# Optimization experiments

Hardware: AMD Instinct MI355X
Metric: run time of the kernel (lower is better)

Reference implementation:

```python
import math
import jax, jax.numpy as jnp
import numpy as np

HIDDEN = 1024   # config.hidden_size
INTER = 4096    # config.intermediate_size
EXPERTS = 8     # config.moe_experts == config.global_experts
B, T = 4, 2048
EPS = 1e-12     # config.epsilon
CAP_FACTOR = 1.0
MIN_CAP = 4


def layer_norm(x, g, b, eps=EPS):
    m = jnp.mean(x, axis=-1, keepdims=True)
    v = jnp.var(x, axis=-1, keepdims=True)
    return (x - m) * jax.lax.rsqrt(v + eps) * g + b


def top1_gate(x, wg, capacity):
    # DeepSpeed top1gating: softmax gate, argmax expert, capacity-based token drop.
    logits = x @ wg                                    # [S, E]
    gates = jax.nn.softmax(logits, axis=-1)
    E = wg.shape[-1]
    idx = jnp.argmax(gates, axis=-1)                   # [S]
    mask1 = jax.nn.one_hot(idx, E, dtype=gates.dtype)  # [S, E]
    locations = jnp.cumsum(mask1, axis=0) - mask1      # exclusive cumsum = slot within expert
    mask1 = mask1 * (locations < capacity).astype(gates.dtype)  # drop overflow tokens
    gates1_s = jnp.sum(gates * mask1, axis=-1)         # [S] prob of chosen expert
    loc_s = jnp.sum(locations * mask1, axis=-1).astype(jnp.int32)
    loc_oh = jax.nn.one_hot(loc_s, capacity, dtype=gates.dtype)          # [S, C]
    combine = gates1_s[:, None, None] * mask1[:, :, None] * loc_oh[:, None, :]  # [S, E, C]
    dispatch = jax.lax.stop_gradient((combine > 0).astype(x.dtype))      # bool mask in torch
    return combine, dispatch


def setup_inputs() -> dict:
    key = jax.random.key(0)
    ks = jax.random.split(key, 8)
    s = 0.02
    return {
        "x": jax.random.normal(ks[0], (B, T, HIDDEN), jnp.float32),
        "attn_nw": jnp.ones((HIDDEN,), jnp.float32),
        "attn_nb": jnp.zeros((HIDDEN,), jnp.float32),
        "wg": jax.random.normal(ks[1], (HIDDEN, EXPERTS), jnp.float32) * s,
        "inter_w": jax.random.normal(ks[2], (EXPERTS, HIDDEN, INTER), jnp.float32) * s,
        "inter_b": jnp.zeros((EXPERTS, INTER), jnp.float32),
        "output_w": jax.random.normal(ks[3], (EXPERTS, INTER, HIDDEN), jnp.float32) * s,
        "output_b": jnp.zeros((EXPERTS, HIDDEN), jnp.float32),
        "res_inter_w": jax.random.normal(ks[4], (HIDDEN, INTER), jnp.float32) * s,
        "res_inter_b": jnp.zeros((INTER,), jnp.float32),
        "res_output_w": jax.random.normal(ks[5], (INTER, HIDDEN), jnp.float32) * s,
        "res_output_b": jnp.zeros((HIDDEN,), jnp.float32),
        "res_coef": jax.random.normal(ks[6], (HIDDEN, 2), jnp.float32) * s,
    }


def reference(x, attn_nw, attn_nb, wg, inter_w, inter_b, output_w, output_b,
              res_inter_w, res_inter_b, res_output_w, res_output_b, res_coef):
    Bx, Tx, M = x.shape
    S = Bx * Tx
    E = wg.shape[-1]
    capacity = max(MIN_CAP, math.ceil(S / E * CAP_FACTOR))  # static

    residual = x.reshape(S, M)                  # attention output + bias (attention = identity here)
    attn_out = layer_norm(residual, attn_nw, attn_nb)  # ds_layernorm

    # gate + dispatch: einsum_sec_sm_ecm
    combine, dispatch = top1_gate(attn_out, wg, capacity)
    dispatched = jnp.einsum('sec,sm->ecm', dispatch, attn_out)  # [E, C, M]

    # expert MLPs: fused gemm-gelu then output projection + bias
    h = jax.nn.gelu(jnp.einsum('ecm,emi->eci', dispatched, inter_w) + inter_b[:, None, :], approximate=True)
    expert_out = jnp.einsum('eci,eim->ecm', h, output_w) + output_b[:, None, :]

    # gated combine: matmul(combine.reshape(S, E*C), expert_out.reshape(E*C, M))
    moe_out = jnp.einsum('sec,ecm->sm', combine, expert_out)

    # residual-MLP branch (mlp_type == 'residual')
    rh = jax.nn.gelu(attn_out @ res_inter_w + res_inter_b, approximate=True)
    res_mlp_out = rh @ res_output_w + res_output_b
    coef = jax.nn.softmax(attn_out @ res_coef, axis=-1)          # [S, 2]
    out = res_mlp_out * coef[:, :1] + moe_out * coef[:, 1:]      # moe_res_matmul

    out = out + residual                                         # bias_residual
    return out.reshape(Bx, Tx, M)
```

## Files before the change

### kernel.cpp

```cpp
#include <hip/hip_runtime.h>
#include <hip/hip_bf16.h>
#include <type_traits>

#define S_TOK 8192
#define HID 1024
#define INTERX 4096
#define NEXP 8
#define CAPX 1024
#define MTOT 16384

using f32x4 = __attribute__((ext_vector_type(4))) float;
using bf16x8 = __attribute__((ext_vector_type(8))) short;

__device__ __forceinline__ short f2bf(float f) {
    union { float f; unsigned u; } v; v.f = f;
    unsigned r = (v.u + 0x7FFFu + ((v.u >> 16) & 1u)) >> 16;
    return (short)r;
}
__device__ __forceinline__ float bflo(int p) {
    union { unsigned u; float f; } v; v.u = (unsigned)p << 16; return v.f;
}
__device__ __forceinline__ float bfhi(int p) {
    union { unsigned u; float f; } v; v.u = (unsigned)p & 0xffff0000u; return v.f;
}

__device__ __forceinline__ float gelu_f(float x) {
    float x2 = x * x;
    float t = __expf(x * fmaf(x2, -0.07135677f, -1.5957691f));
    return x * __builtin_amdgcn_rcpf(1.0f + t);
}

__device__ __forceinline__ void gl_lds16(const short* g, short* l) {
    __builtin_amdgcn_global_load_lds(
        (const __attribute__((address_space(1))) void*)g,
        (__attribute__((address_space(3))) void*)l, 16, 0, 0);
}

template<int PERM>
__device__ __forceinline__ void convtrans_body(
    short (*tile)[72],
    const float* __restrict__ src_e, const float* __restrict__ src_r,
    short* __restrict__ dst, int K, int N, long sSrc, long sDst,
    int bxi, int byi, long z)
{
    const float* s = (z < 8) ? (src_e + z * sSrc) : src_r;
    short* d = dst + z * sDst;
    int n0 = bxi * 64, k0 = byi * 64;
    int t = threadIdx.x;
    int br = t >> 4, bc = t & 15;
    const float* sp = s + (long)(k0 + br * 4) * N + n0 + bc * 4;
    float4 r0 = *(const float4*)(sp);
    float4 r1 = *(const float4*)(sp + N);
    float4 r2 = *(const float4*)(sp + 2 * (long)N);
    float4 r3 = *(const float4*)(sp + 3 * (long)N);
    if (PERM) {
        float rr[4][4] = { {r0.x,r0.y,r0.z,r0.w}, {r1.x,r1.y,r1.z,r1.w},
                           {r2.x,r2.y,r2.z,r2.w}, {r3.x,r3.y,r3.z,r3.w} };
#pragma unroll
        for (int j = 0; j < 4; j++) {
            int kl = br * 4 + j;
            int kp = (kl & 15) * 4 + (kl >> 4);
#pragma unroll
            for (int q = 0; q < 4; q++)
                tile[bc * 4 + q][kp] = f2bf(rr[j][q]);
        }
    } else {
        short4 c0 = { f2bf(r0.x), f2bf(r1.x), f2bf(r2.x), f2bf(r3.x) };
        short4 c1 = { f2bf(r0.y), f2bf(r1.y), f2bf(r2.y), f2bf(r3.y) };
        short4 c2 = { f2bf(r0.z), f2bf(r1.z), f2bf(r2.z), f2bf(r3.z) };
        short4 c3 = { f2bf(r0.w), f2bf(r1.w), f2bf(r2.w), f2bf(r3.w) };
        *(short4*)&tile[bc * 4 + 0][br * 4] = c0;
        *(short4*)&tile[bc * 4 + 1][br * 4] = c1;
        *(short4*)&tile[bc * 4 + 2][br * 4] = c2;
        *(short4*)&tile[bc * 4 + 3][br * 4] = c3;
    }
    __syncthreads();
    int n = t >> 2, kc = (t & 3) * 16;
    int4 o0 = *(const int4*)&tile[n][kc];
    int4 o1 = *(const int4*)&tile[n][kc + 8];
    short* dp = d + (long)(n0 + n) * K + k0 + kc;
    *(int4*)(dp) = o0;
    *(int4*)(dp + 8) = o1;
}

template<int PERM>
__global__ __launch_bounds__(256) void convtrans_kernel(
    const float* __restrict__ src_e, const float* __restrict__ src_r,
    short* __restrict__ dst, int K, int N, long sSrc, long sDst)
{
    __shared__ __align__(16) short tile[64][72];
    convtrans_body<PERM>(tile, src_e, src_r, dst, K, N, sSrc, sDst,
                         blockIdx.x, blockIdx.y, (long)blockIdx.z);
}

__global__ __launch_bounds__(256) void fused_pre_kernel(
    const float* __restrict__ src_e, const float* __restrict__ src_r,
    short* __restrict__ w1t,
    const float* __restrict__ x, const float* __restrict__ nw, const float* __restrict__ nb,
    const float* __restrict__ wg, const float* __restrict__ rcf,
    short* __restrict__ attn_bf, int* __restrict__ eidx, float* __restrict__ gate,
    float* __restrict__ coef0, float* __restrict__ coef1,
    int* __restrict__ map2, int* __restrict__ zbufi)
{
    __shared__ __align__(16) short tile[64][72];
    int z = blockIdx.z;
    if (z < 9) {
        convtrans_body<0>(tile, src_e, src_r, w1t, HID, INTERX,
                          (long)HID * INTERX, (long)HID * INTERX,
                          blockIdx.x, blockIdx.y, (long)z);
        return;
    }
    int s = (z - 9) * 1024 + blockIdx.y * 64 + blockIdx.x;
    int tid = threadIdx.x;
    int lane = tid & 63, wave = tid >> 6;
    double (*gred)[10] = (double(*)[10])(&tile[0][0]);
    float  (*wred)[2]  = (float(*)[2])(&tile[32][0]);

    if (tid == 0) {
        map2[s] = -1;
        map2[NEXP * CAPX + s] = s;
    }
    if (s == 0) ((int2*)zbufi)[tid] = int2{0, 0};

    float4 xv = *(const float4*)(x + (size_t)s * HID + tid * 4);
    float sum = xv.x + xv.y + xv.z + xv.w;
    float sq  = xv.x*xv.x + xv.y*xv.y + xv.z*xv.z + xv.w*xv.w;
#pragma unroll
    for (int o = 32; o > 0; o >>= 1) {
        sum += __shfl_down(sum, o, 64);
        sq  += __shfl_down(sq, o, 64);
    }
    if (lane == 0) { wred[wave][0] = sum; wred[wave][1] = sq; }
    __syncthreads();
    float ts = wred[0][0] + wred[1][0] + wred[2][0] + wred[3][0];
    float tq = wred[0][1] + wred[1][1] + wred[2][1] + wred[3][1];
    float m  = ts * (1.0f / HID);
    float var = tq * (1.0f / HID) - m * m;
    float rs = rsqrtf(var + 1e-12f);

    float4 g4 = *(const float4*)(nw + tid * 4);
    float4 b4 = *(const float4*)(nb + tid * 4);
    float y[4];
    y[0] = (xv.x - m) * rs * g4.x + b4.x;
    y[1] = (xv.y - m) * rs * g4.y + b4.y;
    y[2] = (xv.z - m) * rs * g4.z + b4.z;
    y[3] = (xv.w - m) * rs * g4.w + b4.w;

    short4 yb = { f2bf(y[0]), f2bf(y[1]), f2bf(y[2]), f2bf(y[3]) };
    *(short4*)(attn_bf + (size_t)s * HID + tid * 4) = yb;

    double a[10];
#pragma unroll
    for (int q = 0; q < 10; q++) a[q] = 0.0;
#pragma unroll
    for (int j = 0; j < 4; j++) {
        int k = tid * 4 + j;
        float4 w0 = *(const float4*)(wg + k * 8);
        float4 w1 = *(const float4*)(wg + k * 8 + 4);
        double yj = (double)y[j];
        a[0] += yj * w0.x; a[1] += yj * w0.y; a[2] += yj * w0.z; a[3] += yj * w0.w;
        a[4] += yj * w1.x; a[5] += yj * w1.y; a[6] += yj * w1.z; a[7] += yj * w1.w;
        float2 rc = *(const float2*)(rcf + k * 2);
        a[8] += yj * rc.x; a[9] += yj * rc.y;
    }
#pragma unroll
    for (int o = 32; o > 0; o >>= 1)
#pragma unroll
        for (int q = 0; q < 10; q++) a[q] += __shfl_down(a[q], o, 64);
    if (lane == 0)
#pragma unroll
        for (int q = 0; q < 10; q++) gred[wave][q] = a[q];
    __syncthreads();
    if (tid == 0) {
        float l[8];
#pragma unroll
        for (int e = 0; e < 8; e++)
            l[e] = (float)(gred[0][e] + gred[1][e] + gred[2][e] + gred[3][e]);
        int bi = 0; float bv = l[0];
#pragma unroll
        for (int e = 1; e < 8; e++) if (l[e] > bv) { bv = l[e]; bi = e; }
        float den = 0.0f;
#pragma unroll
        for (int e = 0; e < 8; e++) den += expf(l[e] - bv);
        gate[s] = 1.0f / den;
        eidx[s] = bi;
        float r0 = (float)(gred[0][8] + gred[1][8] + gred[2][8] + gred[3][8]);
        float r1 = (float)(gred[0][9] + gred[1][9] + gred[2][9] + gred[3][9]);
        float mx = fmaxf(r0, r1);
        float e0 = expf(r0 - mx), e1 = expf(r1 - mx);
        float inv = 1.0f / (e0 + e1);
        coef0[s] = e0 * inv; coef1[s] = e1 * inv;
    }
}

__global__ __launch_bounds__(256) void assign_kernel(
    const int* __restrict__ eidx, int* __restrict__ slot, int* __restrict__ map2)
{
    int tid = threadIdx.x;
    __shared__ int se[S_TOK];
    __shared__ int cnt[2][256][NEXP];
#pragma unroll
    for (int i = 0; i < S_TOK / 4 / 256; i++)
        ((int4*)se)[tid + i * 256] = ((const int4*)eidx)[tid + i * 256];
    __syncthreads();

    int c[NEXP];
#pragma unroll
    for (int e = 0; e < NEXP; e++) c[e] = 0;
    int base = tid * 32;
#pragma unroll
    for (int q = 0; q < 8; q++) {
        int4 v = ((const int4*)se)[tid * 8 + q];
        c[v.x]++; c[v.y]++; c[v.z]++; c[v.w]++;
    }
#pragma unroll
    for (int e = 0; e < NEXP; e++) cnt[0][tid][e] = c[e];
    __syncthreads();

    int src = 0;
    for (int step = 1; step < 256; step <<= 1) {
        int dst = src ^ 1;
#pragma unroll
        for (int e = 0; e < NEXP; e++) {
            int v = cnt[src][tid][e];
            if (tid >= step) v += cnt[src][tid - step][e];
            cnt[dst][tid][e] = v;
        }
        __syncthreads();
        src = dst;
    }
    int off[NEXP];
#pragma unroll
    for (int e = 0; e < NEXP; e++) off[e] = (tid > 0) ? cnt[src][tid - 1][e] : 0;
    for (int t = 0; t < 32; t++) {
        int s = base + t;
        int e = se[s];
        int loc = off[e]++;
        if (loc < CAPX) { slot[s] = loc; map2[e * CAPX + loc] = s; }
        else            { slot[s] = -1; }
    }
}

template<int EPI, int GATHER>
__global__ __launch_bounds__(256, 2) void gemm_kernel(
    const short* __restrict__ A, const short* __restrict__ W,
    const float* __restrict__ bias_e, const float* __restrict__ bias_r,
    short* __restrict__ out, const int* __restrict__ map2,
    const short* __restrict__ zbuf, int N, int K, long sW, long sB)
{
    __shared__ __align__(16) short a_lds[128 * 64];
    __shared__ __align__(16) short b_lds[256 * 64];

    int L = blockIdx.x + gridDim.x * blockIdx.y;
    int by = (L & 7) * 16 + ((L >> 3) & 15);
    int bx = L >> 7;

    long e = by >> 3; if (e > 8) e = 8;
    const short* Wb = W + e * sW;
    const float* biasb = (by < 64) ? (bias_e + e * sB) : bias_r;

    int tid = threadIdx.x;
    int lane = tid & 63, wave = tid >> 6;
    int wm = wave & 1, wn = wave >> 1;
    int lm = lane & 15, lq = lane >> 4;
    int lr = lane >> 3, ch = lane & 7;
    int chs = (ch ^ lr) * 8;

    const short* pA[4];
    const short* pB[8];
#pragma unroll
    for (int it = 0; it < 4; it++) {
        int row = (wave * 4 + it) * 8 + lr;
        if (GATHER) {
            int s = map2[by * 128 + row];
            pA[it] = (s >= 0) ? (A + (long)s * K) : zbuf;
        } else {
            pA[it] = A + ((long)by * 128 + row) * K;
        }
    }
#pragma unroll
    for (int it = 0; it < 8; it++) {
        int row = (wave * 8 + it) * 8 + lr;
        pB[it] = Wb + ((long)bx * 256 + row) * K;
    }

    f32x4 acc[4][8];
#pragma unroll
    for (int i = 0; i < 4; i++)
#pragma unroll
        for (int j = 0; j < 8; j++) acc[i][j] = { 0.f, 0.f, 0.f, 0.f };

    for (int kb = 0; kb < K; kb += 64) {
#pragma unroll
        for (int it = 0; it < 4; it++)
            gl_lds16(pA[it] + kb + chs, a_lds + (wave * 4 + it) * 512);
#pragma unroll
        for (int it = 0; it < 8; it++)
            gl_lds16(pB[it] + kb + chs, b_lds + (wave * 8 + it) * 512);
        __syncthreads();
#pragma unroll
        for (int ks = 0; ks < 64; ks += 32) {
            int po = ((lq ^ (lm & 7)) * 8) ^ ks;
            bf16x8 af[4], bfr[8];
#pragma unroll
            for (int i = 0; i < 4; i++)
                af[i] = *(const bf16x8*)(a_lds + (wm * 64 + i * 16 + lm) * 64 + po);
#pragma unroll
            for (int j = 0; j < 8; j++)
                bfr[j] = *(const bf16x8*)(b_lds + (wn * 128 + j * 16 + lm) * 64 + po);
#pragma unroll
            for (int i = 0; i < 4; i++)
#pragma unroll
                for (int j = 0; j < 8; j++)
                    acc[i][j] = __builtin_amdgcn_mfma_f32_16x16x32_bf16(af[i], bfr[j], acc[i][j], 0, 0, 0);
        }
        __syncthreads();
    }

    float bb[8];
#pragma unroll
    for (int j = 0; j < 8; j++)
        bb[j] = biasb[bx * 256 + wn * 128 + j * 16 + lm];

#pragma unroll
    for (int i = 0; i < 4; i++) {
#pragma unroll
        for (int r = 0; r < 4; r++) {
            long row = (long)by * 128 + wm * 64 + i * 16 + lq * 4 + r;
            if (EPI == 1) {
                short* rp = out + row * N + bx * 256 + wn * 128;
#pragma unroll
                for (int h = 0; h < 2; h++) {
                    int b0 = f2bf(gelu_f(acc[i][h*4+0][r] + bb[h*4+0]));
                    int b1 = f2bf(gelu_f(acc[i][h*4+1][r] + bb[h*4+1]));
                    int b2 = f2bf(gelu_f(acc[i][h*4+2][r] + bb[h*4+2]));
                    int b3 = f2bf(gelu_f(acc[i][h*4+3][r] + bb[h*4+3]));
                    int2 pk;
                    pk.x = (b0 & 0xFFFF) | (b1 << 16);
                    pk.y = (b2 & 0xFFFF) | (b3 << 16);
                    *(int2*)(rp + h * 64 + lm * 4) = pk;
                }
            } else {
#pragma unroll
                for (int j = 0; j < 8; j++) {
                    int col = bx * 256 + wn * 128 + j * 16 + lm;
                    out[row * N + col] = f2bf(acc[i][j][r] + bb[j]);
                }
            }
        }
    }
}

__global__ __launch_bounds__(256) void final_kernel(
    const float* __restrict__ x, const short* __restrict__ eout2,
    const int* __restrict__ eidx, const int* __restrict__ slot,
    const float* __restrict__ gate, const float* __restrict__ coef0,
    const float* __restrict__ coef1, float* __restrict__ out)
{
    int s = blockIdx.x, tid = threadIdx.x;
    float c0 = coef0[s], g = gate[s] * coef1[s];
    int sl = slot[s], e = eidx[s];
    float4 xv = *(const float4*)(x + (size_t)s * HID + tid * 4);
    int2 rm = *(const int2*)(eout2 + ((size_t)(NEXP * CAPX + s)) * HID + tid * 4);
    int2 mo = { 0, 0 };
    if (sl >= 0) mo = *(const int2*)(eout2 + ((size_t)(e * CAPX + sl)) * HID + tid * 4);
    float4 o;
    o.x = bflo(rm.x) * c0 + g * bflo(mo.x) + xv.x;
    o.y = bfhi(rm.x) * c0 + g * bfhi(mo.x) + xv.y;
    o.z = bflo(rm.y) * c0 + g * bflo(mo.y) + xv.z;
    o.w = bfhi(rm.y) * c0 + g * bfhi(mo.y) + xv.w;
    *(float4*)(out + (size_t)s * HID + tid * 4) = o;
}

extern "C" void kernel_launch(void* const* d_in, const int* in_sizes, int n_in,
                              void* d_out, int out_size, void* d_ws, size_t ws_size,
                              hipStream_t stream) {
    const float* x           = (const float*)d_in[0];
    const float* attn_nw     = (const float*)d_in[1];
    const float* attn_nb     = (const float*)d_in[2];
    const float* wg          = (const float*)d_in[3];
    const float* inter_w     = (const float*)d_in[4];
    const float* inter_b     = (const float*)d_in[5];
    const float* output_w    = (const float*)d_in[6];
    const float* output_b    = (const float*)d_in[7];
    const float* res_inter_w = (const float*)d_in[8];
    const float* res_inter_b = (const float*)d_in[9];
    const float* res_output_w= (const float*)d_in[10];
    const float* res_output_b= (const float*)d_in[11];
    const float* res_coef    = (const float*)d_in[12];
    float* out = (float*)d_out;

    char* ws = (char*)d_ws;
    size_t off = 0;
    auto alloc = [&](size_t bytes) { void* p = ws + off; off += (bytes + 255) & ~(size_t)255; return p; };
    char* region1 = (char*)alloc((size_t)MTOT * HID * 2);
    short* wreg   = (short*)alloc((size_t)9 * HID * INTERX * 2);
    short* hbuf2  = (short*)alloc((size_t)MTOT * INTERX * 2);
    int*   eidx   = (int*)alloc(S_TOK * 4);
    int*   slot   = (int*)alloc(S_TOK * 4);
    float* gate   = (float*)alloc(S_TOK * 4);
    float* c0     = (float*)alloc(S_TOK * 4);
    float* c1     = (float*)alloc(S_TOK * 4);
    int*   map2   = (int*)alloc(MTOT * 4);
    short* zbuf   = (short*)alloc(1024 * 2);

    short* attn_bf = (short*)region1;
    short* eout2   = (short*)region1;
    short* w1t = wreg;
    short* w2t = wreg;

    fused_pre_kernel<<<dim3(64, 16, 17), 256, 0, stream>>>(
        inter_w, res_inter_w, w1t,
        x, attn_nw, attn_nb, wg, res_coef,
        attn_bf, eidx, gate, c0, c1, map2, (int*)zbuf);

    assign_kernel<<<1, 256, 0, stream>>>(eidx, slot, map2);

    gemm_kernel<1, 1><<<dim3(INTERX/256, 128), 256, 0, stream>>>(
        attn_bf, w1t, inter_b, res_inter_b, hbuf2, map2, zbuf,
        INTERX, HID, (long)HID*INTERX, INTERX);

    convtrans_kernel<1><<<dim3(HID/64, INTERX/64, 9), 256, 0, stream>>>(
        output_w, res_output_w, w2t, INTERX, HID, (long)INTERX*HID, (long)INTERX*HID);

    gemm_kernel<0, 0><<<dim3(HID/256, 128), 256, 0, stream>>>(
        hbuf2, w2t, output_b, res_output_b, eout2, nullptr, zbuf,
        HID, INTERX, (long)INTERX*HID, HID);

    final_kernel<<<S_TOK, 256, 0, stream>>>(x, eout2, eidx, slot, gate, c0, c1, out);

    (void)in_sizes; (void)n_in; (void)out_size; (void)ws_size;
}
```

Before: 731.7 us.

## Fuse second-weight conversion into first GEMM launch via separate workspace buffer

Appends convert/transpose blocks for the output weights to the grid of the first expert GEMM, so the weight conversion runs alongside the tail of GEMM1 instead of as a separate serialized launch. This needs its own buffer for the transposed weights, because the first GEMM still reads the shared weight region. The fused path is used only when the workspace is large enough, otherwise it falls back to the old two-launch sequence. The combined launch uses a 1D grid, and the GEMM blocks still come first in block order.

```diff
diff --git a/kernel.cpp b/kernel.cpp
--- a/kernel.cpp
+++ b/kernel.cpp
@@ -246,12 +246,23 @@
     const short* __restrict__ A, const short* __restrict__ W,
     const float* __restrict__ bias_e, const float* __restrict__ bias_r,
     short* __restrict__ out, const int* __restrict__ map2,
-    const short* __restrict__ zbuf, int N, int K, long sW, long sB)
+    const short* __restrict__ zbuf, int N, int K, long sW, long sB,
+    const float* __restrict__ cw_e, const float* __restrict__ cw_r,
+    short* __restrict__ cdst, int nGemm)
 {
     __shared__ __align__(16) short a_lds[128 * 64];
     __shared__ __align__(16) short b_lds[256 * 64];
 
-    int L = blockIdx.x + gridDim.x * blockIdx.y;
+    int bid = blockIdx.x + gridDim.x * blockIdx.y;
+    if (bid >= nGemm) {
+        int cid = bid - nGemm;
+        convtrans_body<1>((short(*)[72])a_lds, cw_e, cw_r, cdst,
+                          INTERX, HID, (long)INTERX * HID, (long)INTERX * HID,
+                          cid & 15, (cid >> 4) & 63, (long)(cid >> 10));
+        return;
+    }
+
+    int L = bid;
     int by = (L & 7) * 16 + ((L >> 3) & 15);
     int bx = L >> 7;
 
@@ -404,10 +415,15 @@
     int*   map2   = (int*)alloc(MTOT * 4);
     short* zbuf   = (short*)alloc(1024 * 2);
 
+    size_t off_base = off;
+    short* w2t_sep = (short*)alloc((size_t)9 * HID * INTERX * 2);
+    bool sep = (off <= ws_size);
+    short* w2t = sep ? w2t_sep : wreg;
+    if (!sep) off = off_base;
+
     short* attn_bf = (short*)region1;
     short* eout2   = (short*)region1;
     short* w1t = wreg;
-    short* w2t = wreg;
 
     fused_pre_kernel<<<dim3(64, 16, 17), 256, 0, stream>>>(
         inter_w, res_inter_w, w1t,
@@ -416,18 +432,30 @@
 
     assign_kernel<<<1, 256, 0, stream>>>(eidx, slot, map2);
 
-    gemm_kernel<1, 1><<<dim3(INTERX/256, 128), 256, 0, stream>>>(
-        attn_bf, w1t, inter_b, res_inter_b, hbuf2, map2, zbuf,
-        INTERX, HID, (long)HID*INTERX, INTERX);
-
-    convtrans_kernel<1><<<dim3(HID/64, INTERX/64, 9), 256, 0, stream>>>(
-        output_w, res_output_w, w2t, INTERX, HID, (long)INTERX*HID, (long)INTERX*HID);
-
-    gemm_kernel<0, 0><<<dim3(HID/256, 128), 256, 0, stream>>>(
+    const int NG1 = (MTOT / 128) * (INTERX / 256);
+
+    if (sep) {
+        gemm_kernel<1, 1><<<dim3(NG1 + 9216), 256, 0, stream>>>(
+            attn_bf, w1t, inter_b, res_inter_b, hbuf2, map2, zbuf,
+            INTERX, HID, (long)HID*INTERX, INTERX,
+            output_w, res_output_w, w2t, NG1);
+    } else {
+        gemm_kernel<1, 1><<<dim3(NG1), 256, 0, stream>>>(
+            attn_bf, w1t, inter_b, res_inter_b, hbuf2, map2, zbuf,
+            INTERX, HID, (long)HID*INTERX, INTERX,
+            nullptr, nullptr, nullptr, NG1);
+        convtrans_kernel<1><<<dim3(HID/64, INTERX/64, 9), 256, 0, stream>>>(
+            output_w, res_output_w, w2t, INTERX, HID,
+            (long)INTERX*HID, (long)INTERX*HID);
+    }
+
+    const int NG2 = (MTOT / 128) * (HID / 256);
+    gemm_kernel<0, 0><<<dim3(NG2), 256, 0, stream>>>(
         hbuf2, w2t, output_b, res_output_b, eout2, nullptr, zbuf,
-        HID, INTERX, (long)INTERX*HID, HID);
+        HID, INTERX, (long)INTERX*HID, HID,
+        nullptr, nullptr, nullptr, NG2);
 
     final_kernel<<<S_TOK, 256, 0, stream>>>(x, eout2, eidx, slot, gate, c0, c1, out);
 
-    (void)in_sizes; (void)n_in; (void)out_size; (void)ws_size;
-}
+    (void)in_sizes; (void)n_in; (void)out_size;
+}
```

Result: faster. 714.4 us (-2.4%).
